# Kernel optimization log

Hardware: AMD Instinct MI355X
Metric: run time of the kernel (lower is better)

## Reference

```python
import jax, jax.numpy as jnp
import numpy as np
import math

SQRT2 = np.float32(math.sqrt(2.0))
APPROX_FACTOR = np.float32(1.5 / math.sqrt(2.0))
EPS = np.float32(1e-32)

C, F = 4096, 4096  # out_channels, in_features of the quantized weight


def setup_inputs() -> dict:
    key = jax.random.key(0)
    k_x, k_s, k_z, k_l, k_a = jax.random.split(key, 5)
    x = jax.random.normal(k_x, (C, F), dtype=jnp.float32)
    # per-channel positive scale (delta), like scale1 = p in (0, 1]
    scale = jax.random.uniform(k_s, (C, 1), dtype=jnp.float32, minval=0.5, maxval=1.0)
    # element-wise zero-point (integer-valued, stored as float as in torch code)
    zero = jax.random.randint(k_z, (C, F), 0, 4).astype(jnp.float32)
    # code_map: log base per element; exactly sqrt(2) so the hardware-approx
    # equality test (code_map == sqrt(2)) fires, matching 'log_sqrt2'.
    code_map = jnp.full((C, F), SQRT2, dtype=jnp.float32)
    # level_map: number of quantization levels per element (integer-valued float)
    level_map = jax.random.randint(k_l, (C, F), 0, 8).astype(jnp.float32)
    # asym_map: per-channel asymmetry flag in {0, 1}
    asym_map = jax.random.randint(k_a, (C, 1), 0, 2).astype(jnp.float32)
    return {"x": x, "scale": scale, "zero": zero, "code_map": code_map,
            "level_map": level_map, "asym_map": asym_map}


def reference(x, scale, zero, code_map, level_map, asym_map):
    # log_quantize, 'sqrt2' branch, hardware_approx=True
    x_log = jnp.log(jnp.abs(x / scale) + EPS) / jnp.log(code_map)
    x_int = jnp.round(x_log)
    lo = -1.0 - asym_map / 2.0
    x_clamp_1 = jnp.maximum(x_int - zero, lo)            # clamp(min=lo, max=inf)
    x_clamp = jnp.minimum(x_clamp_1 - level_map, -1.0)   # clamp(min=-inf, max=-1)
    e = x_clamp + level_map + zero
    x_quant = jnp.power(code_map, e)
    # hardware approximation: odd sqrt(2)-powers use 1.5/sqrt(2) factor
    sqrt2_flag = (code_map == SQRT2) & (jnp.mod(e, 2.0) != 0.0)
    x_quant = jnp.where(sqrt2_flag, x_quant * APPROX_FACTOR, x_quant)
    s = jnp.sign(x)
    zero_flag = x_clamp_1 <= lo
    x_quant = jnp.where(zero_flag, 0.0, x_quant)
    return x_quant * s * scale
```

## Files before the change

### kernel.cpp

```cpp
#include <hip/hip_runtime.h>
#include <math.h>

#define SQRT2F   1.41421356237309504880f
#define EPSF     1e-32f
#define BTOL     3e-5f

__global__ __launch_bounds__(256) void uaq_kernel(
    const float4* __restrict__ x,
    const float*  __restrict__ scale,
    const float4* __restrict__ zero,
    const float4* __restrict__ code,
    const float4* __restrict__ level,
    const float*  __restrict__ asym,
    float4* __restrict__ out,
    int n4)
{
    int i = blockIdx.x * blockDim.x + threadIdx.x;
    if (i >= n4) return;

    int row = i >> 10;
    float sc = scale[row];
    float lo = -1.0f - 0.5f * asym[row];

    float4 xv = x[i];
    float4 zv = zero[i];
    float4 cv = code[i];
    float4 lv = level[i];
    float4 ov;

    const float* xp = &xv.x;
    const float* zp = &zv.x;
    const float* cp = &cv.x;
    const float* lp = &lv.x;
    float* op = &ov.x;

    #pragma unroll
    for (int k = 0; k < 4; ++k) {
        float xe = xp[k], ze = zp[k], ce = cp[k], le = lp[k];

        float ax  = fabsf(xe / sc);
        float axe = ax + EPSF;

        float xlg = logf(axe) / logf(ce);
        float fr  = xlg - floorf(xlg);
        float xi;
        if (fabsf(fr - 0.5f) < BTOL) {
            float L32 = (float)log((double)axe);
            float D32 = (float)log((double)ce);
            float q32 = L32 / D32;
            xi = rintf(q32);
        } else {
            xi = rintf(xlg);
        }

        float xc1 = fmaxf(xi - ze, lo);
        float xc  = fminf(xc1 - le, -1.0f);
        float e   = xc + le + ze;

        bool  is_s2 = (ce == SQRT2F);
        float q;
        if (is_s2) {
            int ei = (int)e;
            q = (ei & 1) ? ldexpf(1.5f, (ei - 1) >> 1)
                         : ldexpf(1.0f, ei >> 1);
        } else {
            q = powf(ce, e);
        }

        float s = (xe > 0.0f) ? 1.0f : ((xe < 0.0f) ? -1.0f : 0.0f);
        if (xc1 <= lo) q = 0.0f;

        op[k] = q * s * sc;
    }

    out[i] = ov;
}

extern "C" void kernel_launch(void* const* d_in, const int* in_sizes, int n_in,
                              void* d_out, int out_size, void* d_ws, size_t ws_size,
                              hipStream_t stream) {
    const float* x     = (const float*)d_in[0];
    const float* scale = (const float*)d_in[1];
    const float* zero  = (const float*)d_in[2];
    const float* code  = (const float*)d_in[3];
    const float* level = (const float*)d_in[4];
    const float* asym  = (const float*)d_in[5];
    float* out = (float*)d_out;

    int n  = out_size;
    int n4 = n / 4;

    int block = 256;
    int grid  = (n4 + block - 1) / block;

    uaq_kernel<<<grid, block, 0, stream>>>(
        (const float4*)x, scale, (const float4*)zero, (const float4*)code,
        (const float4*)level, asym, (float4*)out, n4);
}
```

Measured before the change: 65.18 us.

## Process eight elements per thread with fast sqrt2 log path and nontemporal stores

Each thread now handles two float4 groups and computes one reciprocal of scale per row. When the code map equals sqrt(2), it uses a fast log2 times two instead of two logf calls and a divide. Outputs are written with nontemporal stores, and the sign handling uses copysign. The slow double-precision tie-breaking path is kept, but the fast intrinsics may move the rounding boundaries slightly.

```diff
diff --git a/kernel.cpp b/kernel.cpp
--- a/kernel.cpp
+++ b/kernel.cpp
@@ -4,6 +4,46 @@
 #define SQRT2F   1.41421356237309504880f
 #define EPSF     1e-32f
 #define BTOL     3e-5f
+
+typedef float floatx4 __attribute__((ext_vector_type(4)));
+
+__device__ __forceinline__ float quant_one(float xe, float ze, float ce, float le,
+                                           float sc, float rsc, float lo)
+{
+    float axe_e = fabsf(xe * rsc) + EPSF;
+    bool  is_s2 = (ce == SQRT2F);
+    float xlg;
+    if (is_s2) {
+        xlg = 2.0f * __log2f(axe_e);
+    } else {
+        xlg = __logf(axe_e) / logf(ce);
+    }
+    float xi = rintf(xlg);
+    float t  = xlg - xi;
+    if (fabsf(fabsf(t) - 0.5f) < BTOL) {
+        float axe = fabsf(xe / sc) + EPSF;
+        float L32 = (float)log((double)axe);
+        float D32 = (float)log((double)ce);
+        xi = rintf(L32 / D32);
+    }
+
+    float xc1 = fmaxf(xi - ze, lo);
+    float xc  = fminf(xc1 - le, -1.0f);
+    float e   = xc + le + ze;
+
+    float q;
+    if (is_s2) {
+        int ei = (int)e;
+        q = (ei & 1) ? ldexpf(1.5f, (ei - 1) >> 1)
+                     : ldexpf(1.0f, ei >> 1);
+    } else {
+        q = powf(ce, e);
+    }
+
+    q = copysignf(q, xe);
+    if (xc1 <= lo) q = 0.0f;
+    return q * sc;
+}
 
 __global__ __launch_bounds__(256) void uaq_kernel(
     const float4* __restrict__ x,
@@ -12,68 +52,31 @@
     const float4* __restrict__ code,
     const float4* __restrict__ level,
     const float*  __restrict__ asym,
-    float4* __restrict__ out,
-    int n4)
+    floatx4* __restrict__ out,
+    int n8)
 {
     int i = blockIdx.x * blockDim.x + threadIdx.x;
-    if (i >= n4) return;
+    if (i >= n8) return;
 
-    int row = i >> 10;
-    float sc = scale[row];
-    float lo = -1.0f - 0.5f * asym[row];
+    int row = i >> 9;
+    float sc  = scale[row];
+    float rsc = 1.0f / sc;
+    float lo  = fmaf(-0.5f, asym[row], -1.0f);
 
-    float4 xv = x[i];
-    float4 zv = zero[i];
-    float4 cv = code[i];
-    float4 lv = level[i];
-    float4 ov;
-
-    const float* xp = &xv.x;
-    const float* zp = &zv.x;
-    const float* cp = &cv.x;
-    const float* lp = &lv.x;
-    float* op = &ov.x;
-
+    int b = i * 2;
     #pragma unroll
-    for (int k = 0; k < 4; ++k) {
-        float xe = xp[k], ze = zp[k], ce = cp[k], le = lp[k];
-
-        float ax  = fabsf(xe / sc);
-        float axe = ax + EPSF;
-
-        float xlg = logf(axe) / logf(ce);
-        float fr  = xlg - floorf(xlg);
-        float xi;
-        if (fabsf(fr - 0.5f) < BTOL) {
-            float L32 = (float)log((double)axe);
-            float D32 = (float)log((double)ce);
-            float q32 = L32 / D32;
-            xi = rintf(q32);
-        } else {
-            xi = rintf(xlg);
-        }
-
-        float xc1 = fmaxf(xi - ze, lo);
-        float xc  = fminf(xc1 - le, -1.0f);
-        float e   = xc + le + ze;
-
-        bool  is_s2 = (ce == SQRT2F);
-        float q;
-        if (is_s2) {
-            int ei = (int)e;
-            q = (ei & 1) ? ldexpf(1.5f, (ei - 1) >> 1)
-                         : ldexpf(1.0f, ei >> 1);
-        } else {
-            q = powf(ce, e);
-        }
-
-        float s = (xe > 0.0f) ? 1.0f : ((xe < 0.0f) ? -1.0f : 0.0f);
-        if (xc1 <= lo) q = 0.0f;
-
-        op[k] = q * s * sc;
+    for (int h = 0; h < 2; ++h) {
+        float4 xv = x[b + h];
+        float4 zv = zero[b + h];
+        float4 cv = code[b + h];
+        float4 lv = level[b + h];
+        floatx4 ov;
+        ov.x = quant_one(xv.x, zv.x, cv.x, lv.x, sc, rsc, lo);
+        ov.y = quant_one(xv.y, zv.y, cv.y, lv.y, sc, rsc, lo);
+        ov.z = quant_one(xv.z, zv.z, cv.z, lv.z, sc, rsc, lo);
+        ov.w = quant_one(xv.w, zv.w, cv.w, lv.w, sc, rsc, lo);
+        __builtin_nontemporal_store(ov, &out[b + h]);
     }
-
-    out[i] = ov;
 }
 
 extern "C" void kernel_launch(void* const* d_in, const int* in_sizes, int n_in,
@@ -88,12 +91,12 @@
     float* out = (float*)d_out;
 
     int n  = out_size;
-    int n4 = n / 4;
+    int n8 = n / 8;
 
     int block = 256;
-    int grid  = (n4 + block - 1) / block;
+    int grid  = (n8 + block - 1) / block;
 
     uaq_kernel<<<grid, block, 0, stream>>>(
         (const float4*)x, scale, (const float4*)zero, (const float4*)code,
-        (const float4*)level, asym, (float4*)out, n4);
+        (const float4*)level, asym, (floatx4*)out, n8);
 }
```

Result: slower. 73.99 us (+13.5%).
